# Performance work log

Measured on AMD Instinct MI355X. Metric: run time of the kernel, lower is better.

## Reference

```python
import jax, jax.numpy as jnp
import numpy as np
import math

N, M, D = 16384, 4096, 256
RATIO = 0.5
EDGE_PROB = 0.005  # ~80 nodes per hyperedge on average


def setup_inputs() -> dict:
    key = jax.random.key(0)
    k0, k1, k2, k3 = jax.random.split(key, 4)
    node_features = jax.random.normal(k0, (N, D), dtype=jnp.float32)
    # sparse-ish 0/1 incidence matrix, stored dense as in the original module
    incidence = (jax.random.uniform(k1, (N, M)) < EDGE_PROB).astype(jnp.float32)
    node_mask = jnp.ones((N,), dtype=bool)
    edge_mask = jnp.ones((M,), dtype=bool)
    W = (jax.random.normal(k2, (D, D)) / np.sqrt(D)).astype(jnp.float32)
    b = jnp.zeros((D,), dtype=jnp.float32)
    proj = (jax.random.normal(k3, (D,)) * 0.01).astype(jnp.float32)
    return dict(node_features=node_features, incidence=incidence,
                node_mask=node_mask, edge_mask=edge_mask,
                W=W, b=b, proj=proj)


def reference(node_features, incidence, node_mask, edge_mask, W, b, proj):
    n = node_features.shape[0]
    k = max(1, math.ceil(RATIO * n))  # static

    # --- UniGCNConv: node -> edge mean, edge -> node mean, then linear ---
    deg_e = jnp.clip(jnp.sum(incidence, axis=0), 1.0)          # [m]
    x_edge = (incidence.T @ node_features) / deg_e[:, None]     # [m, d]
    deg_v = jnp.clip(jnp.sum(incidence, axis=1), 1.0)           # [n]
    agg = (incidence @ x_edge) / deg_v[:, None]                 # [n, d]
    embeddings = agg @ W + b                                    # [n, d]

    # --- learned scalar score per node ---
    scores = jax.nn.sigmoid(embeddings @ proj)                  # [n]
    scores = jnp.where(node_mask, scores, -jnp.inf)

    # --- full argsort top-k -> boolean node mask (as in original) ---
    ranked = jnp.argsort(-scores)
    top_k_indices = ranked[:k]
    new_node_mask = jnp.zeros(n, dtype=jnp.bool_).at[top_k_indices].set(True)

    # --- gate features by score ---
    gated_features = node_features * scores[:, None]            # [n, d]

    # --- incidence masked-reduce -> active edges ---
    active_membership = incidence * new_node_mask[:, None].astype(incidence.dtype)
    edge_active_count = jnp.sum(active_membership, axis=0)      # [m]
    new_edge_mask = (edge_active_count > 0) & edge_mask

    return gated_features, new_node_mask, new_edge_mask
```

## Files before the change

### kernel.cpp

```cpp
#include <hip/hip_runtime.h>
#include <stdint.h>
#include <math.h>

#define N_NODES 16384
#define M_EDGES 4096
#define DFEAT   256
#define KSEL    8192
#define VCAP    96


__global__ void compute_w2(const float* __restrict__ W, const float* __restrict__ b,
                           const float* __restrict__ proj, double* __restrict__ w2,
                           double* __restrict__ bp) {
    int d = threadIdx.x;
    double acc = 0.0;
    for (int j = 0; j < DFEAT; ++j)
        acc += (double)W[d * DFEAT + j] * (double)proj[j];
    w2[d] = acc;
    if (d == 0) {
        double s = 0.0;
        for (int j = 0; j < DFEAT; ++j) s += (double)b[j] * (double)proj[j];
        *bp = s;
    }
}

__global__ void z_kernel(const float* __restrict__ X, const double* __restrict__ w2,
                         double* __restrict__ z) {
    int wave = threadIdx.x >> 6;
    int lane = threadIdx.x & 63;
    int n = blockIdx.x * 4 + wave;
    float4 x = ((const float4*)X)[n * 64 + lane];
    int j = lane * 4;
    double acc = (double)x.x * w2[j] + (double)x.y * w2[j + 1]
               + (double)x.z * w2[j + 2] + (double)x.w * w2[j + 3];
    for (int o = 32; o > 0; o >>= 1) acc += __shfl_down(acc, o, 64);
    if (lane == 0) z[n] = acc;
}

__global__ void build(const float* __restrict__ inc, const double* __restrict__ z,
                      int* __restrict__ ecnt, int* __restrict__ vcnt,
                      double* __restrict__ ysum, uint16_t* __restrict__ vlist) {
    int n = blockIdx.x;
    int t = threadIdx.x;
    int lane = t & 63, wv = t >> 6;
    const float4* row4 = (const float4*)inc + (long long)n * 1024;
    unsigned bits = 0;
#pragma unroll
    for (int c = 0; c < 4; ++c) {
        float4 v = row4[c * 256 + t];
        unsigned b = (v.x != 0.0f ? 1u : 0u) | (v.y != 0.0f ? 2u : 0u)
                   | (v.z != 0.0f ? 4u : 0u) | (v.w != 0.0f ? 8u : 0u);
        bits |= b << (c * 4);
    }
    double zn = z[n];
    unsigned bb = bits;
    while (bb) {
        int k = __ffs(bb) - 1;
        bb &= bb - 1;
        int m = ((k >> 2) << 10) + t * 4 + (k & 3);
        atomicAdd(&ysum[m], zn);
        atomicAdd(&ecnt[m], 1);
    }
    int h = __popc(bits);
    int incl = h;
    for (int o = 1; o < 64; o <<= 1) {
        int v = __shfl_up(incl, o, 64);
        if (lane >= o) incl += v;
    }
    __shared__ int wtot[4];
    if (lane == 63) wtot[wv] = incl;
    __syncthreads();
    int base = incl - h;
#pragma unroll
    for (int w = 0; w < 4; ++w) if (w < wv) base += wtot[w];
    if (t == 0) vcnt[n] = wtot[0] + wtot[1] + wtot[2] + wtot[3];
    uint16_t* vrow = vlist + (long long)n * VCAP;
    int s = base;
    while (bits) {
        int k = __ffs(bits) - 1;
        bits &= bits - 1;
        int m = ((k >> 2) << 10) + t * 4 + (k & 3);
        if (s < VCAP) vrow[s] = (uint16_t)m;
        ++s;
    }
}

__global__ void ymean_kernel(const double* __restrict__ ysum, const int* __restrict__ ecnt,
                             double* __restrict__ ymean) {
    int m = blockIdx.x * blockDim.x + threadIdx.x;
    if (m >= M_EDGES) return;
    int c = ecnt[m];
    ymean[m] = ysum[m] / (c > 0 ? (double)c : 1.0);
}

__global__ void logit_kernel(const double* __restrict__ ymean, const int* __restrict__ vcnt,
                             const uint16_t* __restrict__ vlist, const double* __restrict__ bp,
                             unsigned long long* __restrict__ keys, float* __restrict__ scores) {
    int n = blockIdx.x * blockDim.x + threadIdx.x;
    if (n >= N_NODES) return;
    int cntr = vcnt[n];
    int cnt = cntr > VCAP ? VCAP : cntr;
    const uint16_t* lst = vlist + (long long)n * VCAP;
    double acc = 0.0;
    for (int i = 0; i < cnt; ++i) acc += ymean[lst[i]];
    double deg = cntr > 0 ? (double)cntr : 1.0;
    double logit = acc / deg + *bp;
    scores[n] = (float)(1.0 / (1.0 + exp(-logit)));
    unsigned long long u = (unsigned long long)__double_as_longlong(logit);
    u = (u >> 63) ? ~u : (u | 0x8000000000000000ull);
    keys[n] = u;
}

__global__ __launch_bounds__(1024) void radix_select(
        const unsigned long long* __restrict__ keys, unsigned long long* __restrict__ Tu) {
    int tid = threadIdx.x;
    int wave = tid >> 6, lane = tid & 63;
    unsigned long long k[16];
#pragma unroll
    for (int i = 0; i < 16; ++i) k[i] = keys[i * 1024 + tid];
    __shared__ unsigned long long wsum[2][16];
    unsigned long long prefix = 0ull;
    int kr = KSEL;
    int par = 0;
    for (int shift = 62; shift >= 0; shift -= 2, par ^= 1) {
        unsigned long long base = prefix >> shift;
        int c3 = 0, c2 = 0, c1 = 0;
#pragma unroll
        for (int i = 0; i < 16; ++i) {
            unsigned long long hi = k[i] >> shift;
            c3 += (hi == base + 3);
            c2 += (hi == base + 2);
            c1 += (hi == base + 1);
        }
        unsigned long long packed = (unsigned long long)c3
                                  | ((unsigned long long)c2 << 21)
                                  | ((unsigned long long)c1 << 42);
        for (int o = 32; o > 0; o >>= 1) packed += __shfl_down(packed, o, 64);
        if (lane == 0) wsum[par][wave] = packed;
        __syncthreads();
        unsigned long long tot = 0;
#pragma unroll
        for (int w = 0; w < 16; ++w) tot += wsum[par][w];
        int n3 = (int)(tot & 0x1FFFFF);
        int n2 = (int)((tot >> 21) & 0x1FFFFF);
        int n1 = (int)((tot >> 42) & 0x1FFFFF);
        if (kr <= n3) prefix |= 3ull << shift;
        else { kr -= n3;
            if (kr <= n2) prefix |= 2ull << shift;
            else { kr -= n2;
                if (kr <= n1) prefix |= 1ull << shift;
                else kr -= n1;
            }
        }
    }
    if (tid == 0) *Tu = prefix;
}

__global__ __launch_bounds__(1024) void build_mask(
        const unsigned long long* __restrict__ keys, const unsigned long long* __restrict__ Tu,
        float* __restrict__ out_mask, int* __restrict__ maski) {
    int tid = threadIdx.x;
    int wave = tid >> 6, lane = tid & 63;
    unsigned long long T = *Tu;
    unsigned long long k[16];
#pragma unroll
    for (int i = 0; i < 16; ++i) k[i] = keys[tid * 16 + i];
    int ceq = 0, cgt = 0;
#pragma unroll
    for (int i = 0; i < 16; ++i) { cgt += (k[i] > T); ceq += (k[i] == T); }
    int eq_incl = ceq;
    for (int o = 1; o < 64; o <<= 1) {
        int v = __shfl_up(eq_incl, o, 64);
        if (lane >= o) eq_incl += v;
    }
    int gt_sum = cgt;
    for (int o = 32; o > 0; o >>= 1) gt_sum += __shfl_down(gt_sum, o, 64);
    __shared__ int weq[16], wgt[16];
    if (lane == 63) weq[wave] = eq_incl;
    if (lane == 0)  wgt[wave] = gt_sum;
    __syncthreads();
    int base_eq = 0, tot_gt = 0;
#pragma unroll
    for (int w = 0; w < 16; ++w) {
        if (w < wave) base_eq += weq[w];
        tot_gt += wgt[w];
    }
    int need = KSEL - tot_gt;
    int r = base_eq + eq_incl - ceq;
#pragma unroll
    for (int i = 0; i < 16; ++i) {
        bool eq = (k[i] == T);
        bool sel = (k[i] > T) || (eq && r < need);
        if (eq) ++r;
        int idx = tid * 16 + i;
        out_mask[idx] = sel ? 1.0f : 0.0f;
        maski[idx] = sel ? 1 : 0;
    }
}

__global__ void gated_out(const float* __restrict__ X, const float* __restrict__ scores,
                          float* __restrict__ out) {
    int idx = blockIdx.x * blockDim.x + threadIdx.x;
    int n = idx >> 6;
    float s = scores[n];
    float4 v = ((const float4*)X)[idx];
    v.x *= s; v.y *= s; v.z *= s; v.w *= s;
    ((float4*)out)[idx] = v;
}

__global__ void emask_scatter(const int* __restrict__ maski, const int* __restrict__ vcnt,
                              const uint16_t* __restrict__ vlist, float* __restrict__ out) {
    int n = blockIdx.x * blockDim.x + threadIdx.x;
    if (n >= N_NODES || !maski[n]) return;
    int cntr = vcnt[n];
    int cnt = cntr > VCAP ? VCAP : cntr;
    const uint16_t* lst = vlist + (long long)n * VCAP;
    for (int i = 0; i < cnt; ++i) out[lst[i]] = 1.0f;
}

extern "C" void kernel_launch(void* const* d_in, const int* in_sizes, int n_in,
                              void* d_out, int out_size, void* d_ws, size_t ws_size,
                              hipStream_t stream) {
    const float* X    = (const float*)d_in[0];
    const float* inc  = (const float*)d_in[1];
    const float* W    = (const float*)d_in[4];
    const float* b    = (const float*)d_in[5];
    const float* proj = (const float*)d_in[6];

    char* ws = (char*)d_ws;
    int*                ecnt   = (int*)(ws + 0);
    int*                vcnt   = (int*)(ws + 16384);
    double*             ysum   = (double*)(ws + 81920);
    double*             w2     = (double*)(ws + 114688);
    double*             bp     = (double*)(ws + 116736);
    unsigned long long* Tu     = (unsigned long long*)(ws + 116744);
    unsigned long long* keys   = (unsigned long long*)(ws + 131072);
    float*              scores = (float*)(ws + 262144);
    int*                maski  = (int*)(ws + 327680);
    double*             z      = (double*)(ws + 393216);
    double*             ymean  = (double*)(ws + 524288);
    uint16_t*           vlist  = (uint16_t*)(ws + 557056);

    float* out_gated = (float*)d_out;
    float* out_nmask = out_gated + (long long)N_NODES * DFEAT;
    float* out_emask = out_nmask + N_NODES;

    hipMemsetAsync(ws, 0, 114688, stream);
    hipMemsetAsync(out_emask, 0, M_EDGES * sizeof(float), stream);

    compute_w2<<<1, 256, 0, stream>>>(W, b, proj, w2, bp);
    z_kernel<<<N_NODES / 4, 256, 0, stream>>>(X, w2, z);
    build<<<N_NODES, 256, 0, stream>>>(inc, z, ecnt, vcnt, ysum, vlist);
    ymean_kernel<<<M_EDGES / 256, 256, 0, stream>>>(ysum, ecnt, ymean);
    logit_kernel<<<N_NODES / 256, 256, 0, stream>>>(ymean, vcnt, vlist, bp, keys, scores);
    radix_select<<<1, 1024, 0, stream>>>(keys, Tu);
    build_mask<<<1, 1024, 0, stream>>>(keys, Tu, out_nmask, maski);
    gated_out<<<(N_NODES * DFEAT / 4) / 256, 256, 0, stream>>>(X, scores, out_gated);
    emask_scatter<<<N_NODES / 256, 256, 0, stream>>>(maski, vcnt, vlist, out_emask);
}
```

Baseline: 490.6 us.

## Fuse pipeline kernels and pad per-edge accumulators to cache lines

Folds the per-node z dot product into the build kernel, removes the ymean kernel by dividing inside logit_kernel, merges radix select with mask building in one block, and combines the edge-mask scatter with the gating epilogue. Per-edge sum and count now sit together in a 64-byte padded slot so atomics on different edges do not share a cache line. This cuts kernel launches and intermediate round trips, at the cost of a larger memset and repeated divisions per incidence in logit_kernel. The select kernel now loads keys in a blocked rather than strided order.

```diff
diff --git a/kernel.cpp b/kernel.cpp
--- a/kernel.cpp
+++ b/kernel.cpp
@@ -24,25 +24,19 @@
     }
 }
 
-__global__ void z_kernel(const float* __restrict__ X, const double* __restrict__ w2,
-                         double* __restrict__ z) {
-    int wave = threadIdx.x >> 6;
-    int lane = threadIdx.x & 63;
-    int n = blockIdx.x * 4 + wave;
-    float4 x = ((const float4*)X)[n * 64 + lane];
-    int j = lane * 4;
-    double acc = (double)x.x * w2[j] + (double)x.y * w2[j + 1]
-               + (double)x.z * w2[j + 2] + (double)x.w * w2[j + 3];
-    for (int o = 32; o > 0; o >>= 1) acc += __shfl_down(acc, o, 64);
-    if (lane == 0) z[n] = acc;
-}
-
-__global__ void build(const float* __restrict__ inc, const double* __restrict__ z,
-                      int* __restrict__ ecnt, int* __restrict__ vcnt,
-                      double* __restrict__ ysum, uint16_t* __restrict__ vlist) {
+__global__ void build(const float* __restrict__ inc, const float* __restrict__ X,
+                      const double* __restrict__ w2, char* __restrict__ eacc,
+                      int* __restrict__ vcnt, uint16_t* __restrict__ vlist) {
     int n = blockIdx.x;
     int t = threadIdx.x;
     int lane = t & 63, wv = t >> 6;
+    __shared__ double zred[4];
+    __shared__ int wtot[4];
+
+    double p = (double)X[(long long)n * DFEAT + t] * w2[t];
+    for (int o = 32; o > 0; o >>= 1) p += __shfl_down(p, o, 64);
+    if (lane == 0) zred[wv] = p;
+
     const float4* row4 = (const float4*)inc + (long long)n * 1024;
     unsigned bits = 0;
 #pragma unroll
@@ -52,22 +46,24 @@
                    | (v.z != 0.0f ? 4u : 0u) | (v.w != 0.0f ? 8u : 0u);
         bits |= b << (c * 4);
     }
-    double zn = z[n];
+    __syncthreads();
+    double zn = zred[0] + zred[1] + zred[2] + zred[3];
+
     unsigned bb = bits;
     while (bb) {
         int k = __ffs(bb) - 1;
         bb &= bb - 1;
         int m = ((k >> 2) << 10) + t * 4 + (k & 3);
-        atomicAdd(&ysum[m], zn);
-        atomicAdd(&ecnt[m], 1);
-    }
+        atomicAdd((double*)(eacc + (size_t)m * 64), zn);
+        atomicAdd((int*)(eacc + (size_t)m * 64 + 8), 1);
+    }
+
     int h = __popc(bits);
     int incl = h;
     for (int o = 1; o < 64; o <<= 1) {
         int v = __shfl_up(incl, o, 64);
         if (lane >= o) incl += v;
     }
-    __shared__ int wtot[4];
     if (lane == 63) wtot[wv] = incl;
     __syncthreads();
     int base = incl - h;
@@ -85,15 +81,7 @@
     }
 }
 
-__global__ void ymean_kernel(const double* __restrict__ ysum, const int* __restrict__ ecnt,
-                             double* __restrict__ ymean) {
-    int m = blockIdx.x * blockDim.x + threadIdx.x;
-    if (m >= M_EDGES) return;
-    int c = ecnt[m];
-    ymean[m] = ysum[m] / (c > 0 ? (double)c : 1.0);
-}
-
-__global__ void logit_kernel(const double* __restrict__ ymean, const int* __restrict__ vcnt,
+__global__ void logit_kernel(const char* __restrict__ eacc, const int* __restrict__ vcnt,
                              const uint16_t* __restrict__ vlist, const double* __restrict__ bp,
                              unsigned long long* __restrict__ keys, float* __restrict__ scores) {
     int n = blockIdx.x * blockDim.x + threadIdx.x;
@@ -102,7 +90,12 @@
     int cnt = cntr > VCAP ? VCAP : cntr;
     const uint16_t* lst = vlist + (long long)n * VCAP;
     double acc = 0.0;
-    for (int i = 0; i < cnt; ++i) acc += ymean[lst[i]];
+    for (int i = 0; i < cnt; ++i) {
+        int m = lst[i];
+        double ys = *(const double*)(eacc + (size_t)m * 64);
+        int ec = *(const int*)(eacc + (size_t)m * 64 + 8);
+        acc += ys / (ec > 0 ? (double)ec : 1.0);
+    }
     double deg = cntr > 0 ? (double)cntr : 1.0;
     double logit = acc / deg + *bp;
     scores[n] = (float)(1.0 / (1.0 + exp(-logit)));
@@ -111,13 +104,15 @@
     keys[n] = u;
 }
 
-__global__ __launch_bounds__(1024) void radix_select(
-        const unsigned long long* __restrict__ keys, unsigned long long* __restrict__ Tu) {
+__global__ __launch_bounds__(1024) void select_mask(
+        const unsigned long long* __restrict__ keys,
+        float* __restrict__ out_mask, int* __restrict__ maski) {
     int tid = threadIdx.x;
     int wave = tid >> 6, lane = tid & 63;
     unsigned long long k[16];
 #pragma unroll
-    for (int i = 0; i < 16; ++i) k[i] = keys[i * 1024 + tid];
+    for (int i = 0; i < 16; ++i) k[i] = keys[tid * 16 + i];
+
     __shared__ unsigned long long wsum[2][16];
     unsigned long long prefix = 0ull;
     int kr = KSEL;
@@ -153,18 +148,8 @@
             }
         }
     }
-    if (tid == 0) *Tu = prefix;
-}
-
-__global__ __launch_bounds__(1024) void build_mask(
-        const unsigned long long* __restrict__ keys, const unsigned long long* __restrict__ Tu,
-        float* __restrict__ out_mask, int* __restrict__ maski) {
-    int tid = threadIdx.x;
-    int wave = tid >> 6, lane = tid & 63;
-    unsigned long long T = *Tu;
-    unsigned long long k[16];
-#pragma unroll
-    for (int i = 0; i < 16; ++i) k[i] = keys[tid * 16 + i];
+    unsigned long long T = prefix;
+
     int ceq = 0, cgt = 0;
 #pragma unroll
     for (int i = 0; i < 16; ++i) { cgt += (k[i] > T); ceq += (k[i] == T); }
@@ -198,24 +183,26 @@
     }
 }
 
-__global__ void gated_out(const float* __restrict__ X, const float* __restrict__ scores,
-                          float* __restrict__ out) {
-    int idx = blockIdx.x * blockDim.x + threadIdx.x;
+__global__ void epilogue(const float* __restrict__ X, const float* __restrict__ scores,
+                         const int* __restrict__ maski, const int* __restrict__ vcnt,
+                         const uint16_t* __restrict__ vlist,
+                         float* __restrict__ out_gated, float* __restrict__ out_emask) {
+    int t = threadIdx.x;
+    int idx = blockIdx.x * 256 + t;
     int n = idx >> 6;
     float s = scores[n];
     float4 v = ((const float4*)X)[idx];
     v.x *= s; v.y *= s; v.z *= s; v.w *= s;
-    ((float4*)out)[idx] = v;
-}
-
-__global__ void emask_scatter(const int* __restrict__ maski, const int* __restrict__ vcnt,
-                              const uint16_t* __restrict__ vlist, float* __restrict__ out) {
-    int n = blockIdx.x * blockDim.x + threadIdx.x;
-    if (n >= N_NODES || !maski[n]) return;
-    int cntr = vcnt[n];
-    int cnt = cntr > VCAP ? VCAP : cntr;
-    const uint16_t* lst = vlist + (long long)n * VCAP;
-    for (int i = 0; i < cnt; ++i) out[lst[i]] = 1.0f;
+    ((float4*)out_gated)[idx] = v;
+    if (blockIdx.x < 64) {
+        int n2 = blockIdx.x * 256 + t;
+        if (maski[n2]) {
+            int cntr = vcnt[n2];
+            int cnt = cntr > VCAP ? VCAP : cntr;
+            const uint16_t* lst = vlist + (long long)n2 * VCAP;
+            for (int i = 0; i < cnt; ++i) out_emask[lst[i]] = 1.0f;
+        }
+    }
 }
 
 extern "C" void kernel_launch(void* const* d_in, const int* in_sizes, int n_in,
@@ -228,33 +215,26 @@
     const float* proj = (const float*)d_in[6];
 
     char* ws = (char*)d_ws;
-    int*                ecnt   = (int*)(ws + 0);
-    int*                vcnt   = (int*)(ws + 16384);
-    double*             ysum   = (double*)(ws + 81920);
-    double*             w2     = (double*)(ws + 114688);
-    double*             bp     = (double*)(ws + 116736);
-    unsigned long long* Tu     = (unsigned long long*)(ws + 116744);
-    unsigned long long* keys   = (unsigned long long*)(ws + 131072);
-    float*              scores = (float*)(ws + 262144);
-    int*                maski  = (int*)(ws + 327680);
-    double*             z      = (double*)(ws + 393216);
-    double*             ymean  = (double*)(ws + 524288);
-    uint16_t*           vlist  = (uint16_t*)(ws + 557056);
+    char*               eacc   = ws + 0;
+    double*             w2     = (double*)(ws + 262144);
+    double*             bp     = (double*)(ws + 264192);
+    unsigned long long* keys   = (unsigned long long*)(ws + 270336);
+    float*              scores = (float*)(ws + 401408);
+    int*                maski  = (int*)(ws + 466944);
+    int*                vcnt   = (int*)(ws + 532480);
+    uint16_t*           vlist  = (uint16_t*)(ws + 598016);
 
     float* out_gated = (float*)d_out;
     float* out_nmask = out_gated + (long long)N_NODES * DFEAT;
     float* out_emask = out_nmask + N_NODES;
 
-    hipMemsetAsync(ws, 0, 114688, stream);
+    hipMemsetAsync(eacc, 0, 262144, stream);
     hipMemsetAsync(out_emask, 0, M_EDGES * sizeof(float), stream);
 
     compute_w2<<<1, 256, 0, stream>>>(W, b, proj, w2, bp);
-    z_kernel<<<N_NODES / 4, 256, 0, stream>>>(X, w2, z);
-    build<<<N_NODES, 256, 0, stream>>>(inc, z, ecnt, vcnt, ysum, vlist);
-    ymean_kernel<<<M_EDGES / 256, 256, 0, stream>>>(ysum, ecnt, ymean);
-    logit_kernel<<<N_NODES / 256, 256, 0, stream>>>(ymean, vcnt, vlist, bp, keys, scores);
-    radix_select<<<1, 1024, 0, stream>>>(keys, Tu);
-    build_mask<<<1, 1024, 0, stream>>>(keys, Tu, out_nmask, maski);
-    gated_out<<<(N_NODES * DFEAT / 4) / 256, 256, 0, stream>>>(X, scores, out_gated);
-    emask_scatter<<<N_NODES / 256, 256, 0, stream>>>(maski, vcnt, vlist, out_emask);
-}
+    build<<<N_NODES, 256, 0, stream>>>(inc, X, w2, eacc, vcnt, vlist);
+    logit_kernel<<<N_NODES / 256, 256, 0, stream>>>(eacc, vcnt, vlist, bp, keys, scores);
+    select_mask<<<1, 1024, 0, stream>>>(keys, out_nmask, maski);
+    epilogue<<<(N_NODES * DFEAT / 4) / 256, 256, 0, stream>>>(X, scores, maski, vcnt, vlist,
+                                                              out_gated, out_emask);
+}
```

Result: no change. 487.5 us (-0.6%).
